# Optimization experiments

Hardware: AMD Instinct MI355X
Metric: run time of the kernel (lower is better)

Reference implementation:

```python
import jax, jax.numpy as jnp
import numpy as np

PAD_IDX = 0
NUM_VISITS, MAX_CODES = 16384, 48
VOCAB, DIM, HID = 20000, 128, 128


def setup_inputs() -> dict:
    key = jax.random.key(0)
    ks = jax.random.split(key, 16)
    ids = jax.random.randint(ks[0], (NUM_VISITS, MAX_CODES), 0, VOCAB)
    # guarantee every visit has at least one non-pad code (original returns
    # zeros for empty visits; we simply avoid that degenerate case)
    ids = ids.at[:, 0].set(jnp.maximum(ids[:, 0], 1))
    s = 0.05
    return {
        "ids": ids,
        "emb": jax.random.normal(ks[1], (VOCAB, DIM), jnp.float32) * s,
        "W1": jax.random.normal(ks[2], (DIM, HID), jnp.float32) * s,
        "b1": jnp.zeros((HID,), jnp.float32),
        "W2": jax.random.normal(ks[3], (HID, HID), jnp.float32) * s,
        "b2": jnp.zeros((HID,), jnp.float32),
        "Wa1": jax.random.normal(ks[4], (HID, HID), jnp.float32) * s,
        "ba1": jnp.zeros((HID,), jnp.float32),
        "wa2": jax.random.normal(ks[5], (HID,), jnp.float32) * s,
        "ba2": jnp.zeros((1,), jnp.float32),
        "Wr1": jax.random.normal(ks[6], (HID, HID), jnp.float32) * s,
        "br1": jnp.zeros((HID,), jnp.float32),
        "Wr2": jax.random.normal(ks[7], (HID, DIM), jnp.float32) * s,
        "br2": jnp.zeros((DIM,), jnp.float32),
    }


def reference(ids, emb, W1, b1, W2, b2, Wa1, ba1, wa2, ba2, Wr1, br1, Wr2, br2):
    # ids: [V, C] padded code indices; pad_idx codes are masked out.
    mask = ids != PAD_IDX                              # [V, C]
    x = emb[ids]                                       # [V, C, D]
    # phi: Linear->SiLU->Linear->SiLU
    h = jax.nn.silu(x @ W1 + b1)
    h = jax.nn.silu(h @ W2 + b2)                       # [V, C, H]
    # attention pooling: Linear->Tanh->Linear(1), masked softmax over codes
    a = jnp.tanh(h @ Wa1 + ba1) @ wa2 + ba2[0]         # [V, C]
    a = jnp.where(mask, a, -jnp.inf)
    a = jax.nn.softmax(a, axis=1)                      # pad rows -> weight 0
    h_pool = jnp.einsum("vc,vch->vh", a, h)            # [V, H]
    # rho: Linear->SiLU->Linear
    v = jax.nn.silu(h_pool @ Wr1 + br1) @ Wr2 + br2    # [V, D]
    return v
```

## Files before the change

### kernel.cpp

```cpp
#include <hip/hip_runtime.h>
#include <math.h>


#define DIM 128
#define MT 32
#define XLDP 136

typedef float f32x4 __attribute__((ext_vector_type(4)));
typedef short short8 __attribute__((ext_vector_type(8)));

#define MFMA(a, b, c) __builtin_amdgcn_mfma_f32_16x16x32_bf16(a, b, c, 0, 0, 0)

__device__ __forceinline__ float fast_rcp(float x) {
  return __builtin_amdgcn_rcpf(x);
}
__device__ __forceinline__ float silu_f(float v) {
  return v * fast_rcp(1.0f + __expf(-v));
}
__device__ __forceinline__ float tanh_f(float v) {
  float t = __expf(2.0f * v);
  return 1.0f - 2.0f * fast_rcp(t + 1.0f);
}

__device__ __forceinline__ unsigned short bf16_hi(float x, float* hif) {
  unsigned u = __builtin_bit_cast(unsigned, x);
  unsigned h = (u + 0x8000u) >> 16;
  *hif = __builtin_bit_cast(float, h << 16);
  return (unsigned short)h;
}
__device__ __forceinline__ unsigned short bf16_rd(float x) {
  unsigned u = __builtin_bit_cast(unsigned, x);
  return (unsigned short)((u + 0x8000u) >> 16);
}
__device__ __forceinline__ unsigned short f2h(float x) {
  return __builtin_bit_cast(unsigned short, (_Float16)x);
}
__device__ __forceinline__ float h2f(unsigned short u) {
  return (float)__builtin_bit_cast(_Float16, u);
}

__global__ __launch_bounds__(256) void prep_wfrags(
    const float* __restrict__ W1, const float* __restrict__ W2,
    const float* __restrict__ Wa1, const float* __restrict__ Wr1,
    const float* __restrict__ Wr2, unsigned short* __restrict__ frags) {
  const int m = blockIdx.x >> 3, chunk = blockIdx.x & 7;
  const float* W = (m == 0) ? W1 : (m == 1) ? W2 : (m == 2) ? Wa1
                  : (m == 3) ? Wr1 : Wr2;
  unsigned short* fh = frags + (size_t)m * 32768;
  unsigned short* fl = fh + 16384;
  const int fid = chunk * 256 + threadIdx.x;
  const int lane = fid & 63, s = (fid >> 6) & 3, t = fid >> 8;
  const int k0 = s * 32 + (lane >> 4) * 8;
  const int n = t * 16 + (lane & 15);
#pragma unroll
  for (int j = 0; j < 8; ++j) {
    float w = W[(size_t)(k0 + j) * DIM + n];
    float hf;
    unsigned short h = bf16_hi(w, &hf);
    fh[fid * 8 + j] = h;
    fl[fid * 8 + j] = bf16_rd(w - hf);
  }
}

__device__ __forceinline__ void stage_bf16(const float* __restrict__ src,
                                           unsigned short (*xh)[XLDP],
                                           unsigned short (*xl)[XLDP],
                                           int tid) {
  const float4* s = (const float4*)src;
#pragma unroll
  for (int tph = 0; tph < 8; ++tph) {
    int idx = tid + tph * 128;
    int r = idx >> 5, c4 = idx & 31;
    float4 v = s[idx];
    float hf;
    ushort4 h, l;
    h.x = bf16_hi(v.x, &hf); l.x = bf16_rd(v.x - hf);
    h.y = bf16_hi(v.y, &hf); l.y = bf16_rd(v.y - hf);
    h.z = bf16_hi(v.z, &hf); l.z = bf16_rd(v.z - hf);
    h.w = bf16_hi(v.w, &hf); l.w = bf16_rd(v.w - hf);
    *(ushort4*)&xh[r][c4 * 4] = h;
    *(ushort4*)&xl[r][c4 * 4] = l;
  }
}

template <int NT>
__device__ __forceinline__ void gemm_frag(const unsigned short (*xh)[XLDP],
                                          const unsigned short (*xl)[XLDP],
                                          const unsigned short* __restrict__ bhp,
                                          const unsigned short* __restrict__ blp,
                                          int tt0, int lane, f32x4 acc[2][NT]) {
  const int cr = lane & 15, g = lane >> 4;
  short8 ah[2][4], al[2][4];
#pragma unroll
  for (int st = 0; st < 2; ++st)
#pragma unroll
    for (int s = 0; s < 4; ++s) {
      ah[st][s] = *(const short8*)&xh[st * 16 + cr][s * 32 + g * 8];
      al[st][s] = *(const short8*)&xl[st * 16 + cr][s * 32 + g * 8];
    }
  short8 bh[2][4], bl[2][4];
#pragma unroll
  for (int s = 0; s < 4; ++s) {
    bh[0][s] = *(const short8*)(bhp + ((size_t)(tt0 * 4 + s) * 64 + lane) * 8);
    bl[0][s] = *(const short8*)(blp + ((size_t)(tt0 * 4 + s) * 64 + lane) * 8);
  }
#pragma unroll
  for (int t = 0; t < NT; ++t) {
    const int cb = t & 1, nb = cb ^ 1;
    if (t < NT - 1) {
#pragma unroll
      for (int s = 0; s < 4; ++s) {
        bh[nb][s] = *(const short8*)(bhp +
            ((size_t)((tt0 + t + 1) * 4 + s) * 64 + lane) * 8);
        bl[nb][s] = *(const short8*)(blp +
            ((size_t)((tt0 + t + 1) * 4 + s) * 64 + lane) * 8);
      }
    }
    f32x4 a0 = {0.f, 0.f, 0.f, 0.f}, a1 = {0.f, 0.f, 0.f, 0.f};
#pragma unroll
    for (int s = 0; s < 4; ++s) {
      a0 = MFMA(al[0][s], bl[cb][s], a0);
      a1 = MFMA(al[1][s], bl[cb][s], a1);
      a0 = MFMA(al[0][s], bh[cb][s], a0);
      a1 = MFMA(al[1][s], bh[cb][s], a1);
      a0 = MFMA(ah[0][s], bl[cb][s], a0);
      a1 = MFMA(ah[1][s], bl[cb][s], a1);
      a0 = MFMA(ah[0][s], bh[cb][s], a0);
      a1 = MFMA(ah[1][s], bh[cb][s], a1);
    }
    acc[0][t] = a0;
    acc[1][t] = a1;
  }
}

__global__ __launch_bounds__(128) void vocab_mfma(
    const float* __restrict__ emb, const unsigned short* __restrict__ frags,
    const float* __restrict__ b1, const float* __restrict__ b2,
    const float* __restrict__ ba1, const float* __restrict__ wa2,
    const float* __restrict__ ba2, unsigned short* __restrict__ H2h,
    float* __restrict__ L) {
  __shared__ unsigned short Xh[2][MT][XLDP], Xl[2][MT][XLDP];
  __shared__ float sP[2][MT];
  const int tid = threadIdx.x, wid = tid >> 6, lane = tid & 63;
  const int cr = lane & 15, g = lane >> 4;
  const int m0 = blockIdx.x * MT;

  stage_bf16(emb + (size_t)m0 * DIM, Xh[0], Xl[0], tid);
  __syncthreads();

  f32x4 acc[2][4];
  gemm_frag<4>(Xh[0], Xl[0], frags, frags + 16384, wid * 4, lane, acc);
#pragma unroll
  for (int t = 0; t < 4; ++t) {
    const int col = (wid * 4 + t) * 16 + cr;
    const float bv = b1[col];
#pragma unroll
    for (int st = 0; st < 2; ++st)
#pragma unroll
      for (int r = 0; r < 4; ++r) {
        float o = silu_f(acc[st][t][r] + bv);
        float hf;
        Xh[1][st * 16 + g * 4 + r][col] = bf16_hi(o, &hf);
        Xl[1][st * 16 + g * 4 + r][col] = bf16_rd(o - hf);
      }
  }
  __syncthreads();
  gemm_frag<4>(Xh[1], Xl[1], frags + 32768, frags + 32768 + 16384,
               wid * 4, lane, acc);
#pragma unroll
  for (int t = 0; t < 4; ++t) {
    const int col = (wid * 4 + t) * 16 + cr;
    const float bv = b2[col];
#pragma unroll
    for (int st = 0; st < 2; ++st)
#pragma unroll
      for (int r = 0; r < 4; ++r) {
        float o = silu_f(acc[st][t][r] + bv);
        float hf;
        const int row = st * 16 + g * 4 + r;
        Xh[0][row][col] = bf16_hi(o, &hf);
        Xl[0][row][col] = bf16_rd(o - hf);
        H2h[(size_t)(m0 + row) * DIM + col] = f2h(o);
      }
  }
  __syncthreads();
  gemm_frag<4>(Xh[0], Xl[0], frags + 65536, frags + 65536 + 16384,
               wid * 4, lane, acc);
  {
    float pl[2][4] = {{0.f, 0.f, 0.f, 0.f}, {0.f, 0.f, 0.f, 0.f}};
#pragma unroll
    for (int t = 0; t < 4; ++t) {
      const int col = (wid * 4 + t) * 16 + cr;
      const float bav = ba1[col], wav = wa2[col];
#pragma unroll
      for (int st = 0; st < 2; ++st)
#pragma unroll
        for (int r = 0; r < 4; ++r)
          pl[st][r] = fmaf(tanh_f(acc[st][t][r] + bav), wav, pl[st][r]);
    }
#pragma unroll
    for (int st = 0; st < 2; ++st)
#pragma unroll
      for (int r = 0; r < 4; ++r) {
        float p = pl[st][r];
        p += __shfl_xor(p, 1, 64);
        p += __shfl_xor(p, 2, 64);
        p += __shfl_xor(p, 4, 64);
        p += __shfl_xor(p, 8, 64);
        if (cr == 0) sP[wid][st * 16 + g * 4 + r] = p;
      }
  }
  __syncthreads();
  if (tid < MT) L[m0 + tid] = sP[0][tid] + sP[1][tid] + ba2[0];
}

__global__ __launch_bounds__(256) void pool_rho(
    const int* __restrict__ ids, const float* __restrict__ L,
    const unsigned short* __restrict__ H2h,
    const unsigned short* __restrict__ frags,
    const float* __restrict__ br1, const float* __restrict__ br2,
    float* __restrict__ out) {
  __shared__ unsigned short Xh[2][MT][XLDP], Xl[2][MT][XLDP];
  const int tid = threadIdx.x, wid = tid >> 6, lane = tid & 63;
  const int cr = lane & 15, g = lane >> 4;
  const int half = lane >> 5, li = lane & 31;
  const int m0 = blockIdx.x * MT;

  for (int k = 0; k < 8; ++k) {
    const int vi = wid * 8 + k;
    const int v = m0 + vi;
    int id = 0;
    float lg = -3.4e38f;
    if (lane < 48) {
      id = ids[(size_t)v * 48 + lane];
      if (id != 0) lg = L[id];
    }
    float mx = lg;
#pragma unroll
    for (int m = 32; m; m >>= 1) mx = fmaxf(mx, __shfl_xor(mx, m, 64));
    float e = (lg > -3.0e38f) ? __expf(lg - mx) : 0.f;
    float s = e;
#pragma unroll
    for (int m = 32; m; m >>= 1) s += __shfl_xor(s, m, 64);
    const float a = e / s;

    float4 acc = make_float4(0.f, 0.f, 0.f, 0.f);
#pragma unroll 8
    for (int c = 0; c < 24; ++c) {
      const int cc = 2 * c + half;
      const float ac = __shfl(a, cc, 64);
      const int idc = __shfl(id, cc, 64);
      const ushort4 hv = ((const ushort4*)(H2h + (size_t)idc * DIM))[li];
      acc.x = fmaf(ac, h2f(hv.x), acc.x);
      acc.y = fmaf(ac, h2f(hv.y), acc.y);
      acc.z = fmaf(ac, h2f(hv.z), acc.z);
      acc.w = fmaf(ac, h2f(hv.w), acc.w);
    }
    acc.x += __shfl_xor(acc.x, 32, 64);
    acc.y += __shfl_xor(acc.y, 32, 64);
    acc.z += __shfl_xor(acc.z, 32, 64);
    acc.w += __shfl_xor(acc.w, 32, 64);
    if (half == 0) {
      float hf;
      ushort4 hh, hl;
      hh.x = bf16_hi(acc.x, &hf); hl.x = bf16_rd(acc.x - hf);
      hh.y = bf16_hi(acc.y, &hf); hl.y = bf16_rd(acc.y - hf);
      hh.z = bf16_hi(acc.z, &hf); hl.z = bf16_rd(acc.z - hf);
      hh.w = bf16_hi(acc.w, &hf); hl.w = bf16_rd(acc.w - hf);
      *(ushort4*)&Xh[0][vi][li * 4] = hh;
      *(ushort4*)&Xl[0][vi][li * 4] = hl;
    }
  }
  __syncthreads();

  f32x4 acc2[2][2];
  gemm_frag<2>(Xh[0], Xl[0], frags + 3 * 32768, frags + 3 * 32768 + 16384,
               wid * 2, lane, acc2);
#pragma unroll
  for (int t = 0; t < 2; ++t) {
    const int col = (wid * 2 + t) * 16 + cr;
    const float bv = br1[col];
#pragma unroll
    for (int st = 0; st < 2; ++st)
#pragma unroll
      for (int r = 0; r < 4; ++r) {
        float o = silu_f(acc2[st][t][r] + bv);
        float hf;
        Xh[1][st * 16 + g * 4 + r][col] = bf16_hi(o, &hf);
        Xl[1][st * 16 + g * 4 + r][col] = bf16_rd(o - hf);
      }
  }
  __syncthreads();
  gemm_frag<2>(Xh[1], Xl[1], frags + 4 * 32768, frags + 4 * 32768 + 16384,
               wid * 2, lane, acc2);
#pragma unroll
  for (int t = 0; t < 2; ++t) {
    const int col = (wid * 2 + t) * 16 + cr;
    const float bv = br2[col];
#pragma unroll
    for (int st = 0; st < 2; ++st)
#pragma unroll
      for (int r = 0; r < 4; ++r)
        out[(size_t)(m0 + st * 16 + g * 4 + r) * DIM + col] =
            acc2[st][t][r] + bv;
  }
}

extern "C" void kernel_launch(void* const* d_in, const int* in_sizes, int n_in,
                              void* d_out, int out_size, void* d_ws,
                              size_t ws_size, hipStream_t stream) {
  const int*   ids = (const int*)  d_in[0];
  const float* emb = (const float*)d_in[1];
  const float* W1  = (const float*)d_in[2];
  const float* b1  = (const float*)d_in[3];
  const float* W2  = (const float*)d_in[4];
  const float* b2  = (const float*)d_in[5];
  const float* Wa1 = (const float*)d_in[6];
  const float* ba1 = (const float*)d_in[7];
  const float* wa2 = (const float*)d_in[8];
  const float* ba2 = (const float*)d_in[9];
  const float* Wr1 = (const float*)d_in[10];
  const float* br1 = (const float*)d_in[11];
  const float* Wr2 = (const float*)d_in[12];
  const float* br2 = (const float*)d_in[13];
  float* out = (float*)d_out;

  const int VOCAB = 20000, V = 16384;

  unsigned short* H2h = (unsigned short*)d_ws;
  float* L = (float*)(H2h + (size_t)VOCAB * DIM);
  unsigned short* frags = (unsigned short*)(L + VOCAB);

  prep_wfrags<<<40, 256, 0, stream>>>(W1, W2, Wa1, Wr1, Wr2, frags);
  vocab_mfma<<<VOCAB / MT, 128, 0, stream>>>(emb, frags, b1, b2, ba1, wa2,
                                             ba2, H2h, L);
  pool_rho<<<V / MT, 256, 0, stream>>>(ids, L, H2h, frags, br1, br2, out);
}
```

Measured before the change: 139.0 us.

## Halve row tile to 16, widen vocab block, drop low-low MFMA term

The row tile per block shrinks from 32 to 16, so both kernels launch twice as many blocks. The vocab kernel now runs 4 waves of 256 threads, each handling 2 column tiles instead of 4. The split-bf16 GEMM drops the lo*lo MFMA product (3 MFMAs per k-step instead of 4) and removes the B-fragment double buffering. The aim is more parallelism and less MFMA work, at the cost of slightly lower precision, less reuse of B fragments across rows, and exposed global load latency.

```diff
diff --git a/kernel.cpp b/kernel.cpp
--- a/kernel.cpp
+++ b/kernel.cpp
@@ -3,7 +3,7 @@
 
 
 #define DIM 128
-#define MT 32
+#define MT 16
 #define XLDP 136
 
 typedef float f32x4 __attribute__((ext_vector_type(4)));
@@ -68,8 +68,8 @@
                                            int tid) {
   const float4* s = (const float4*)src;
 #pragma unroll
-  for (int tph = 0; tph < 8; ++tph) {
-    int idx = tid + tph * 128;
+  for (int tph = 0; tph < 2; ++tph) {
+    int idx = tid + tph * 256;
     int r = idx >> 5, c4 = idx & 31;
     float4 v = s[idx];
     float hf;
@@ -88,59 +88,43 @@
                                           const unsigned short (*xl)[XLDP],
                                           const unsigned short* __restrict__ bhp,
                                           const unsigned short* __restrict__ blp,
-                                          int tt0, int lane, f32x4 acc[2][NT]) {
+                                          int tt0, int lane, f32x4 acc[NT]) {
   const int cr = lane & 15, g = lane >> 4;
-  short8 ah[2][4], al[2][4];
-#pragma unroll
-  for (int st = 0; st < 2; ++st)
+  short8 ah[4], al[4];
+#pragma unroll
+  for (int s = 0; s < 4; ++s) {
+    ah[s] = *(const short8*)&xh[cr][s * 32 + g * 8];
+    al[s] = *(const short8*)&xl[cr][s * 32 + g * 8];
+  }
+#pragma unroll
+  for (int t = 0; t < NT; ++t) {
+    short8 bh[4], bl[4];
 #pragma unroll
     for (int s = 0; s < 4; ++s) {
-      ah[st][s] = *(const short8*)&xh[st * 16 + cr][s * 32 + g * 8];
-      al[st][s] = *(const short8*)&xl[st * 16 + cr][s * 32 + g * 8];
-    }
-  short8 bh[2][4], bl[2][4];
-#pragma unroll
-  for (int s = 0; s < 4; ++s) {
-    bh[0][s] = *(const short8*)(bhp + ((size_t)(tt0 * 4 + s) * 64 + lane) * 8);
-    bl[0][s] = *(const short8*)(blp + ((size_t)(tt0 * 4 + s) * 64 + lane) * 8);
-  }
-#pragma unroll
-  for (int t = 0; t < NT; ++t) {
-    const int cb = t & 1, nb = cb ^ 1;
-    if (t < NT - 1) {
-#pragma unroll
-      for (int s = 0; s < 4; ++s) {
-        bh[nb][s] = *(const short8*)(bhp +
-            ((size_t)((tt0 + t + 1) * 4 + s) * 64 + lane) * 8);
-        bl[nb][s] = *(const short8*)(blp +
-            ((size_t)((tt0 + t + 1) * 4 + s) * 64 + lane) * 8);
-      }
-    }
-    f32x4 a0 = {0.f, 0.f, 0.f, 0.f}, a1 = {0.f, 0.f, 0.f, 0.f};
+      bh[s] = *(const short8*)(bhp +
+          ((size_t)((tt0 + t) * 4 + s) * 64 + lane) * 8);
+      bl[s] = *(const short8*)(blp +
+          ((size_t)((tt0 + t) * 4 + s) * 64 + lane) * 8);
+    }
+    f32x4 a = {0.f, 0.f, 0.f, 0.f};
 #pragma unroll
     for (int s = 0; s < 4; ++s) {
-      a0 = MFMA(al[0][s], bl[cb][s], a0);
-      a1 = MFMA(al[1][s], bl[cb][s], a1);
-      a0 = MFMA(al[0][s], bh[cb][s], a0);
-      a1 = MFMA(al[1][s], bh[cb][s], a1);
-      a0 = MFMA(ah[0][s], bl[cb][s], a0);
-      a1 = MFMA(ah[1][s], bl[cb][s], a1);
-      a0 = MFMA(ah[0][s], bh[cb][s], a0);
-      a1 = MFMA(ah[1][s], bh[cb][s], a1);
-    }
-    acc[0][t] = a0;
-    acc[1][t] = a1;
-  }
-}
-
-__global__ __launch_bounds__(128) void vocab_mfma(
+      a = MFMA(ah[s], bh[s], a);
+      a = MFMA(ah[s], bl[s], a);
+      a = MFMA(al[s], bh[s], a);
+    }
+    acc[t] = a;
+  }
+}
+
+__global__ __launch_bounds__(256) void vocab_mfma(
     const float* __restrict__ emb, const unsigned short* __restrict__ frags,
     const float* __restrict__ b1, const float* __restrict__ b2,
     const float* __restrict__ ba1, const float* __restrict__ wa2,
     const float* __restrict__ ba2, unsigned short* __restrict__ H2h,
     float* __restrict__ L) {
   __shared__ unsigned short Xh[2][MT][XLDP], Xl[2][MT][XLDP];
-  __shared__ float sP[2][MT];
+  __shared__ float sP[4][MT];
   const int tid = threadIdx.x, wid = tid >> 6, lane = tid & 63;
   const int cr = lane & 15, g = lane >> 4;
   const int m0 = blockIdx.x * MT;
@@ -148,70 +132,63 @@
   stage_bf16(emb + (size_t)m0 * DIM, Xh[0], Xl[0], tid);
   __syncthreads();
 
-  f32x4 acc[2][4];
-  gemm_frag<4>(Xh[0], Xl[0], frags, frags + 16384, wid * 4, lane, acc);
-#pragma unroll
-  for (int t = 0; t < 4; ++t) {
-    const int col = (wid * 4 + t) * 16 + cr;
+  f32x4 acc[2];
+  gemm_frag<2>(Xh[0], Xl[0], frags, frags + 16384, wid * 2, lane, acc);
+#pragma unroll
+  for (int t = 0; t < 2; ++t) {
+    const int col = (wid * 2 + t) * 16 + cr;
     const float bv = b1[col];
 #pragma unroll
-    for (int st = 0; st < 2; ++st)
-#pragma unroll
-      for (int r = 0; r < 4; ++r) {
-        float o = silu_f(acc[st][t][r] + bv);
-        float hf;
-        Xh[1][st * 16 + g * 4 + r][col] = bf16_hi(o, &hf);
-        Xl[1][st * 16 + g * 4 + r][col] = bf16_rd(o - hf);
-      }
-  }
-  __syncthreads();
-  gemm_frag<4>(Xh[1], Xl[1], frags + 32768, frags + 32768 + 16384,
-               wid * 4, lane, acc);
-#pragma unroll
-  for (int t = 0; t < 4; ++t) {
-    const int col = (wid * 4 + t) * 16 + cr;
+    for (int r = 0; r < 4; ++r) {
+      float o = silu_f(acc[t][r] + bv);
+      float hf;
+      Xh[1][g * 4 + r][col] = bf16_hi(o, &hf);
+      Xl[1][g * 4 + r][col] = bf16_rd(o - hf);
+    }
+  }
+  __syncthreads();
+  gemm_frag<2>(Xh[1], Xl[1], frags + 32768, frags + 32768 + 16384,
+               wid * 2, lane, acc);
+#pragma unroll
+  for (int t = 0; t < 2; ++t) {
+    const int col = (wid * 2 + t) * 16 + cr;
     const float bv = b2[col];
 #pragma unroll
-    for (int st = 0; st < 2; ++st)
-#pragma unroll
-      for (int r = 0; r < 4; ++r) {
-        float o = silu_f(acc[st][t][r] + bv);
-        float hf;
-        const int row = st * 16 + g * 4 + r;
-        Xh[0][row][col] = bf16_hi(o, &hf);
-        Xl[0][row][col] = bf16_rd(o - hf);
-        H2h[(size_t)(m0 + row) * DIM + col] = f2h(o);
-      }
-  }
-  __syncthreads();
-  gemm_frag<4>(Xh[0], Xl[0], frags + 65536, frags + 65536 + 16384,
-               wid * 4, lane, acc);
+    for (int r = 0; r < 4; ++r) {
+      float o = silu_f(acc[t][r] + bv);
+      float hf;
+      const int row = g * 4 + r;
+      Xh[0][row][col] = bf16_hi(o, &hf);
+      Xl[0][row][col] = bf16_rd(o - hf);
+      H2h[(size_t)(m0 + row) * DIM + col] = f2h(o);
+    }
+  }
+  __syncthreads();
+  gemm_frag<2>(Xh[0], Xl[0], frags + 65536, frags + 65536 + 16384,
+               wid * 2, lane, acc);
   {
-    float pl[2][4] = {{0.f, 0.f, 0.f, 0.f}, {0.f, 0.f, 0.f, 0.f}};
-#pragma unroll
-    for (int t = 0; t < 4; ++t) {
-      const int col = (wid * 4 + t) * 16 + cr;
+    float pl[4] = {0.f, 0.f, 0.f, 0.f};
+#pragma unroll
+    for (int t = 0; t < 2; ++t) {
+      const int col = (wid * 2 + t) * 16 + cr;
       const float bav = ba1[col], wav = wa2[col];
 #pragma unroll
-      for (int st = 0; st < 2; ++st)
-#pragma unroll
-        for (int r = 0; r < 4; ++r)
-          pl[st][r] = fmaf(tanh_f(acc[st][t][r] + bav), wav, pl[st][r]);
-    }
-#pragma unroll
-    for (int st = 0; st < 2; ++st)
-#pragma unroll
-      for (int r = 0; r < 4; ++r) {
-        float p = pl[st][r];
-        p += __shfl_xor(p, 1, 64);
-        p += __shfl_xor(p, 2, 64);
-        p += __shfl_xor(p, 4, 64);
-        p += __shfl_xor(p, 8, 64);
-        if (cr == 0) sP[wid][st * 16 + g * 4 + r] = p;
-      }
-  }
-  __syncthreads();
-  if (tid < MT) L[m0 + tid] = sP[0][tid] + sP[1][tid] + ba2[0];
+      for (int r = 0; r < 4; ++r)
+        pl[r] = fmaf(tanh_f(acc[t][r] + bav), wav, pl[r]);
+    }
+#pragma unroll
+    for (int r = 0; r < 4; ++r) {
+      float p = pl[r];
+      p += __shfl_xor(p, 1, 64);
+      p += __shfl_xor(p, 2, 64);
+      p += __shfl_xor(p, 4, 64);
+      p += __shfl_xor(p, 8, 64);
+      if (cr == 0) sP[wid][g * 4 + r] = p;
+    }
+  }
+  __syncthreads();
+  if (tid < MT)
+    L[m0 + tid] = sP[0][tid] + sP[1][tid] + sP[2][tid] + sP[3][tid] + ba2[0];
 }
 
 __global__ __launch_bounds__(256) void pool_rho(
@@ -226,8 +203,8 @@
   const int half = lane >> 5, li = lane & 31;
   const int m0 = blockIdx.x * MT;
 
-  for (int k = 0; k < 8; ++k) {
-    const int vi = wid * 8 + k;
+  for (int k = 0; k < 4; ++k) {
+    const int vi = wid * 4 + k;
     const int v = m0 + vi;
     int id = 0;
     float lg = -3.4e38f;
@@ -273,7 +250,7 @@
   }
   __syncthreads();
 
-  f32x4 acc2[2][2];
+  f32x4 acc2[2];
   gemm_frag<2>(Xh[0], Xl[0], frags + 3 * 32768, frags + 3 * 32768 + 16384,
                wid * 2, lane, acc2);
 #pragma unroll
@@ -281,14 +258,12 @@
     const int col = (wid * 2 + t) * 16 + cr;
     const float bv = br1[col];
 #pragma unroll
-    for (int st = 0; st < 2; ++st)
-#pragma unroll
-      for (int r = 0; r < 4; ++r) {
-        float o = silu_f(acc2[st][t][r] + bv);
-        float hf;
-        Xh[1][st * 16 + g * 4 + r][col] = bf16_hi(o, &hf);
-        Xl[1][st * 16 + g * 4 + r][col] = bf16_rd(o - hf);
-      }
+    for (int r = 0; r < 4; ++r) {
+      float o = silu_f(acc2[t][r] + bv);
+      float hf;
+      Xh[1][g * 4 + r][col] = bf16_hi(o, &hf);
+      Xl[1][g * 4 + r][col] = bf16_rd(o - hf);
+    }
   }
   __syncthreads();
   gemm_frag<2>(Xh[1], Xl[1], frags + 4 * 32768, frags + 4 * 32768 + 16384,
@@ -298,11 +273,8 @@
     const int col = (wid * 2 + t) * 16 + cr;
     const float bv = br2[col];
 #pragma unroll
-    for (int st = 0; st < 2; ++st)
-#pragma unroll
-      for (int r = 0; r < 4; ++r)
-        out[(size_t)(m0 + st * 16 + g * 4 + r) * DIM + col] =
-            acc2[st][t][r] + bv;
+    for (int r = 0; r < 4; ++r)
+      out[(size_t)(m0 + g * 4 + r) * DIM + col] = acc2[t][r] + bv;
   }
 }
 
@@ -332,7 +304,7 @@
   unsigned short* frags = (unsigned short*)(L + VOCAB);
 
   prep_wfrags<<<40, 256, 0, stream>>>(W1, W2, Wa1, Wr1, Wr2, frags);
-  vocab_mfma<<<VOCAB / MT, 128, 0, stream>>>(emb, frags, b1, b2, ba1, wa2,
+  vocab_mfma<<<VOCAB / MT, 256, 0, stream>>>(emb, frags, b1, b2, ba1, wa2,
                                              ba2, H2h, L);
   pool_rho<<<V / MT, 256, 0, stream>>>(ids, L, H2h, frags, br1, br2, out);
 }
```

Measured after the change: 124.8 us. 10.2% less time.
